# Performance work log

Hardware: AMD Instinct MI355X
Metric: run time of the kernel (lower is better)

The kernel has to match this reference:

```python
import jax, jax.numpy as jnp
import numpy as np

B, T, C = 4, 2048, 1024
H = 16
HD = C // H  # 64
OBS_DIM, ACT_DIM = 17, 6
JOINED_DIM = OBS_DIM + ACT_DIM + 2  # 25


def _make_mask():
    # tril causal mask with every (JOINED_DIM-1 + k*JOINED_DIM)-th column zeroed (RL branch)
    m = np.tril(np.ones((T, T), dtype=np.float32))
    m[:, JOINED_DIM - 1::JOINED_DIM] = 0.0
    return jnp.asarray(m > 0)  # bool [T, T]


MASK = _make_mask()


def setup_inputs() -> dict:
    key = jax.random.key(0)
    ks = jax.random.split(key, 9)
    s = 1.0 / np.sqrt(C)
    return {
        "x": jax.random.normal(ks[0], (B, T, C), dtype=jnp.float32),
        "Wq": jax.random.normal(ks[1], (C, C), dtype=jnp.float32) * s,
        "bq": jax.random.normal(ks[2], (C,), dtype=jnp.float32) * s,
        "Wk": jax.random.normal(ks[3], (C, C), dtype=jnp.float32) * s,
        "bk": jax.random.normal(ks[4], (C,), dtype=jnp.float32) * s,
        "Wv": jax.random.normal(ks[5], (C, C), dtype=jnp.float32) * s,
        "bv": jax.random.normal(ks[6], (C,), dtype=jnp.float32) * s,
        "Wp": jax.random.normal(ks[7], (C, C), dtype=jnp.float32) * s,
        "bp": jax.random.normal(ks[8], (C,), dtype=jnp.float32) * s,
    }


def reference(x, Wq, bq, Wk, bk, Wv, bv, Wp, bp):
    # torch nn.Linear: y = x @ W.T + b
    def split_heads(t):  # [B,T,C] -> [B,H,T,HD]
        return t.reshape(B, T, H, HD).transpose(0, 2, 1, 3)

    q = split_heads(x @ Wq.T + bq)
    k = split_heads(x @ Wk.T + bk)
    v = split_heads(x @ Wv.T + bv)

    att = jnp.einsum("bhqd,bhkd->bhqk", q, k) * (1.0 / np.sqrt(HD))
    att = jnp.where(MASK[None, None, :, :], att, -jnp.inf)
    att = jax.nn.softmax(att, axis=-1)
    # dropout layers are identity in eval mode

    y = jnp.einsum("bhqk,bhkd->bhqd", att, v)  # [B,H,T,HD]
    y = y.transpose(0, 2, 1, 3).reshape(B, T, C)
    return y @ Wp.T + bp
```

## Files before the change

### kernel.cpp

```cpp
#include <hip/hip_runtime.h>
#include <hip/hip_bf16.h>


typedef __attribute__((ext_vector_type(8))) short short8;
typedef __attribute__((ext_vector_type(4))) float floatx4;
typedef unsigned short us;

__device__ __forceinline__ us f2bf(float f){
    union { __hip_bfloat16 h; us u; } cv;
    cv.h = __float2bfloat16(f);
    return cv.u;
}

__device__ __forceinline__ void ld_g2l16(const void* g, void* l){
    __builtin_amdgcn_global_load_lds((const __attribute__((address_space(1))) void*)g,
                                     (__attribute__((address_space(3))) void*)l, 16, 0, 0);
}

__global__ __launch_bounds__(256) void cvt_kernel(const float* __restrict__ in,
                                                  us* __restrict__ out, int n4){
    int i = blockIdx.x * 256 + threadIdx.x;
    if (i < n4){
        float4 v = reinterpret_cast<const float4*>(in)[i];
        ushort4 o;
        o.x = f2bf(v.x); o.y = f2bf(v.y); o.z = f2bf(v.z); o.w = f2bf(v.w);
        reinterpret_cast<ushort4*>(out)[i] = o;
    }
}

__global__ __launch_bounds__(256) void cvt4_kernel(const float* __restrict__ w0, const float* __restrict__ w1,
                                                   const float* __restrict__ w2, const float* __restrict__ w3,
                                                   us* __restrict__ o0, us* __restrict__ o1,
                                                   us* __restrict__ o2, us* __restrict__ o3){
    int wsel = blockIdx.x >> 10;
    int i = (blockIdx.x & 1023) * 256 + threadIdx.x;
    const float* src = (wsel == 0) ? w0 : (wsel == 1) ? w1 : (wsel == 2) ? w2 : w3;
    us* dst = (wsel == 0) ? o0 : (wsel == 1) ? o1 : (wsel == 2) ? o2 : o3;
    float4 v = reinterpret_cast<const float4*>(src)[i];
    ushort4 o;
    o.x = f2bf(v.x); o.y = f2bf(v.y); o.z = f2bf(v.z); o.w = f2bf(v.w);
    reinterpret_cast<ushort4*>(dst)[i] = o;
}


#define QSCALE 0.1803368801111244f

#define BAR() __builtin_amdgcn_s_barrier()
#define LGKM0() do { asm volatile("s_waitcnt lgkmcnt(0)" ::: "memory"); __builtin_amdgcn_sched_barrier(0); } while(0)
#define VMC6() asm volatile("s_waitcnt vmcnt(6)" ::: "memory")
#define VMC0() asm volatile("s_waitcnt vmcnt(0)" ::: "memory")

#define STAGE_A3(buf, kt) do { \
    _Pragma("unroll") \
    for (int c_ = 0; c_ < 4; c_++) \
        ld_g2l16(A + (size_t)(m0 + srow[c_])*1024 + (kt)*64 + sgr[c_]*8, \
                 &smem[(buf)*24576 + (c_*8 + wave)*512]); \
} while(0)

#define STAGE_B3(buf, kt) do { \
    _Pragma("unroll") \
    for (int c_ = 0; c_ < 2; c_++) \
        ld_g2l16(Wb + (size_t)(n0 + srow[c_])*1024 + (kt)*64 + sgr[c_]*8, \
                 &smem[(buf)*24576 + 16384 + (c_*8 + wave)*512]); \
} while(0)

#define LOAD_AF3(buf, IH) do { \
    _Pragma("unroll") \
    for (int i_ = 0; i_ < 4; i_++){ \
        int ra_ = wm*128 + (IH)*64 + i_*16 + lane15; \
        _Pragma("unroll") \
        for (int ks_ = 0; ks_ < 2; ks_++){ \
            int ga_ = (ks_*4 + quad) ^ (ra_ & 7); \
            af[i_][ks_] = *reinterpret_cast<const short8*>(&smem[(buf)*24576 + ra_*64 + ga_*8]); \
        } } \
} while(0)

#define LOAD_BF3(buf) do { \
    _Pragma("unroll") \
    for (int j_ = 0; j_ < 2; j_++){ \
        int rb_ = wn*32 + j_*16 + lane15; \
        _Pragma("unroll") \
        for (int ks_ = 0; ks_ < 2; ks_++){ \
            int gb_ = (ks_*4 + quad) ^ (rb_ & 7); \
            bf[j_][ks_] = *reinterpret_cast<const short8*>(&smem[(buf)*24576 + 16384 + rb_*64 + gb_*8]); \
        } } \
} while(0)

#define MFMA_PH3(IH) do { \
    __builtin_amdgcn_s_setprio(1); \
    _Pragma("unroll") \
    for (int ks_ = 0; ks_ < 2; ks_++) \
        _Pragma("unroll") \
        for (int i_ = 0; i_ < 4; i_++) \
            _Pragma("unroll") \
            for (int j_ = 0; j_ < 2; j_++) \
                acc[(IH)*4 + i_][j_] = __builtin_amdgcn_mfma_f32_16x16x32_bf16( \
                    af[i_][ks_], bf[j_][ks_], acc[(IH)*4 + i_][j_], 0, 0, 0); \
    __builtin_amdgcn_s_setprio(0); \
} while(0)

__global__ __launch_bounds__(512, 2) void gemm_qkv3(
    const us* __restrict__ A,
    const us* __restrict__ Wqb, const us* __restrict__ Wkb, const us* __restrict__ Wvb,
    const float* __restrict__ bq, const float* __restrict__ bk, const float* __restrict__ bv,
    us* __restrict__ qo, us* __restrict__ ko, us* __restrict__ vto)
{
    __shared__ us smem[73728];
    const int tid = threadIdx.x;
    const int lane = tid & 63;
    const int wave = tid >> 6;
    const int lane15 = lane & 15;
    const int quad = lane >> 4;
    const int wm = wave >> 2;
    const int wn = wave & 3;
    const int seg = blockIdx.x >> 3;
    const int n0 = (blockIdx.x & 7) * 128;
    const int m0 = blockIdx.y * 256;

    const us* Wb = (seg == 0) ? Wqb : (seg == 1) ? Wkb : Wvb;
    const float* bias = (seg == 0) ? bq : (seg == 1) ? bk : bv;

    int srow[4], sgr[4];
    #pragma unroll
    for (int c = 0; c < 4; c++){
        int s = (c*8 + wave)*64 + lane;
        srow[c] = s >> 3;
        sgr[c] = (s & 7) ^ ((s >> 3) & 7);
    }

    floatx4 zero = {0.f, 0.f, 0.f, 0.f};
    floatx4 acc[8][2];
    #pragma unroll
    for (int i = 0; i < 8; i++)
        #pragma unroll
        for (int j = 0; j < 2; j++) acc[i][j] = zero;
    short8 af[4][2];
    short8 bf[2][2];

    STAGE_A3(0, 0); STAGE_B3(0, 0);
    STAGE_A3(1, 1); STAGE_B3(1, 1);
    VMC6(); BAR();

    #pragma unroll
    for (int t = 0; t < 16; t++){
        const int cur = t % 3, nxt = (t + 2) % 3;
        LOAD_AF3(cur, 0); LOAD_BF3(cur);
        if (t < 14) STAGE_A3(nxt, t + 2);
        BAR(); LGKM0();
        MFMA_PH3(0);
        BAR();
        LOAD_AF3(cur, 1);
        if (t < 14) STAGE_B3(nxt, t + 2);
        BAR(); LGKM0();
        MFMA_PH3(1);
        if (t < 14) { VMC6(); } else { VMC0(); }
        BAR();
    }

    if (seg < 2){
        #pragma unroll
        for (int i = 0; i < 8; i++){
            #pragma unroll
            for (int j = 0; j < 2; j++){
                int n = n0 + wn*32 + j*16 + lane15;
                float bvv = bias[n];
                #pragma unroll
                for (int r = 0; r < 4; r++){
                    int m = m0 + wm*128 + i*16 + quad*4 + r;
                    float val = acc[i][j][r] + bvv;
                    if (seg == 0){
                        qo[(size_t)m*1024 + n] = f2bf(val * QSCALE);
                    } else {
                        int b = m >> 11, tt = m & 2047;
                        int h = n >> 6,  d = n & 63;
                        ko[(((size_t)b*16 + h)*2048 + tt)*64 + d] = f2bf(val);
                    }
                }
            }
        }
    } else {
        us* lCT = smem;
        const int b = m0 >> 11;
        const int t0 = m0 & 2047;
        #pragma unroll
        for (int j = 0; j < 2; j++){
            int nl = wn*32 + j*16 + lane15;
            float bvv = bias[n0 + nl];
            #pragma unroll
            for (int i = 0; i < 8; i++){
                int ml = wm*128 + i*16 + quad*4;
                unsigned int lo = (unsigned int)f2bf(acc[i][j][0] + bvv) |
                                  ((unsigned int)f2bf(acc[i][j][1] + bvv) << 16);
                unsigned int hi = (unsigned int)f2bf(acc[i][j][2] + bvv) |
                                  ((unsigned int)f2bf(acc[i][j][3] + bvv) << 16);
                uint2 pk2; pk2.x = lo; pk2.y = hi;
                *reinterpret_cast<uint2*>(&lCT[(size_t)nl*264 + ml]) = pk2;
            }
        }
        __syncthreads();
        int nl = tid >> 2;
        int c4 = tid & 3;
        int nC = n0 + nl;
        int h = nC >> 6, d = nC & 63;
        us* dst = vto + (((size_t)b*16 + h)*64 + d)*2048 + t0 + c4*64;
        #pragma unroll
        for (int ii = 0; ii < 8; ii++){
            uint4 v = *reinterpret_cast<const uint4*>(&lCT[(size_t)nl*264 + c4*64 + ii*8]);
            *reinterpret_cast<uint4*>(dst + ii*8) = v;
        }
    }
}

__device__ __forceinline__ void pstore_rg(
    floatx4 (&s)[4], us* pw, bool diag, int rgrow, int j0, int jr, const int (&res)[4],
    int lane15, int quad)
{
    #pragma unroll
    for (int tj = 0; tj < 4; tj++){
        bool bad = (res[tj] + jr) == 24;
        #pragma unroll
        for (int r = 0; r < 4; r++){
            float p = __builtin_amdgcn_exp2f(s[tj][r]);
            bool kill = bad || (diag && (j0 + tj*16 + lane15 > rgrow + quad*4 + r));
            pw[(quad*4 + r)*72 + tj*16 + lane15] = f2bf(kill ? 0.f : p);
        }
    }
}

__global__ __launch_bounds__(256, 3) void flash_attn(
    const us* __restrict__ q,
    const us* __restrict__ k,
    const us* __restrict__ vT,
    us* __restrict__ y)
{
    __shared__ us lK[2][64*64];
    __shared__ us lV[2][64*64];
    __shared__ us lP[4][2][16*72];
    const int tid = threadIdx.x;
    const int lane = tid & 63;
    const int wave = tid >> 6;
    const int lane15 = lane & 15;
    const int quad = lane >> 4;
    const int lin = blockIdx.x;
    const int qt2 = 15 - (lin >> 6);
    const int bh = lin & 63;
    const int b = bh >> 4, h = bh & 15;
    const int rg0 = qt2*128 + wave*16;
    const int rg1 = rg0 + 64;
    const int nIter = 2*qt2 + 2;

    const us* kb = k  + (size_t)bh*2048*64;
    const us* vb = vT + (size_t)bh*64*2048;

    const us* q0 = q + ((size_t)b*2048 + rg0 + lane15)*1024 + h*64 + quad*8;
    const us* q1 = q + ((size_t)b*2048 + rg1 + lane15)*1024 + h*64 + quad*8;
    short8 qf0a = *reinterpret_cast<const short8*>(q0);
    short8 qf0b = *reinterpret_cast<const short8*>(q0 + 32);
    short8 qf1a = *reinterpret_cast<const short8*>(q1);
    short8 qf1b = *reinterpret_cast<const short8*>(q1 + 32);

    floatx4 zero = {0.f, 0.f, 0.f, 0.f};
    floatx4 acc0[4], acc1[4];
    #pragma unroll
    for (int d = 0; d < 4; d++){ acc0[d] = zero; acc1[d] = zero; }
    floatx4 lacc0 = zero, lacc1 = zero;

    us* pw0 = &lP[wave][0][0];
    us* pw1 = &lP[wave][1][0];

    short8 onesb;
    #pragma unroll
    for (int e = 0; e < 8; e++) onesb[e] = (short)0x3F80;

    int res[4];
    #pragma unroll
    for (int tj = 0; tj < 4; tj++) res[tj] = (tj*16 + lane15) % 25;
    int jr = 0;

    int srow[2], sgr[2];
    #pragma unroll
    for (int i = 0; i < 2; i++){
        int s = (i*4 + wave)*64 + lane;
        srow[i] = s >> 3;
        sgr[i] = (s & 7) ^ ((s >> 3) & 7);
    }

    #pragma unroll
    for (int i = 0; i < 2; i++){
        ld_g2l16(kb + (size_t)srow[i]*64 + sgr[i]*8, &lK[0][(i*4 + wave)*512]);
        ld_g2l16(vb + (size_t)srow[i]*2048 + sgr[i]*8, &lV[0][(i*4 + wave)*512]);
    }

    for (int it = 0; it < nIter; it++){
        const int j0 = it*64;
        __syncthreads();

        if (it + 1 < nIter){
            #pragma unroll
            for (int i = 0; i < 2; i++){
                ld_g2l16(kb + (size_t)(j0 + 64 + srow[i])*64 + sgr[i]*8,
                         &lK[(it + 1) & 1][(i*4 + wave)*512]);
                ld_g2l16(vb + (size_t)srow[i]*2048 + j0 + 64 + sgr[i]*8,
                         &lV[(it + 1) & 1][(i*4 + wave)*512]);
            }
        }

        const us* Kb = lK[it & 1];
        const us* Vb = lV[it & 1];
        const bool act0  = (it + 1 < nIter);
        const bool diag0 = (it + 2 == nIter);
        const bool diag1 = (it + 1 == nIter);

        floatx4 s0[4], s1[4];
        #pragma unroll
        for (int tj = 0; tj < 4; tj++){
            int rk = tj*16 + lane15;
            short8 kf0 = *reinterpret_cast<const short8*>(&Kb[rk*64 + ((quad     ^ (rk & 7)))*8]);
            short8 kf1 = *reinterpret_cast<const short8*>(&Kb[rk*64 + (((4+quad) ^ (rk & 7)))*8]);
            floatx4 z1 = __builtin_amdgcn_mfma_f32_16x16x32_bf16(qf1a, kf0, zero, 0, 0, 0);
            s1[tj]     = __builtin_amdgcn_mfma_f32_16x16x32_bf16(qf1b, kf1, z1,   0, 0, 0);
            if (act0){
                floatx4 z0 = __builtin_amdgcn_mfma_f32_16x16x32_bf16(qf0a, kf0, zero, 0, 0, 0);
                s0[tj]     = __builtin_amdgcn_mfma_f32_16x16x32_bf16(qf0b, kf1, z0,   0, 0, 0);
            }
        }

        pstore_rg(s1, pw1, diag1, rg1, j0, jr, res, lane15, quad);
        if (act0)
            pstore_rg(s0, pw0, diag0, rg0, j0, jr, res, lane15, quad);

        #pragma unroll
        for (int ks = 0; ks < 2; ks++){
            short8 pf1 = *reinterpret_cast<const short8*>(&pw1[lane15*72 + ks*32 + quad*8]);
            short8 pf0 = *reinterpret_cast<const short8*>(&pw0[lane15*72 + ks*32 + quad*8]);
            lacc1 = __builtin_amdgcn_mfma_f32_16x16x32_bf16(pf1, onesb, lacc1, 0, 0, 0);
            if (act0) lacc0 = __builtin_amdgcn_mfma_f32_16x16x32_bf16(pf0, onesb, lacc0, 0, 0, 0);
            #pragma unroll
            for (int dt = 0; dt < 4; dt++){
                int rv = dt*16 + lane15;
                short8 vf = *reinterpret_cast<const short8*>(&Vb[rv*64 + (((ks*4+quad) ^ (rv & 7)))*8]);
                acc1[dt] = __builtin_amdgcn_mfma_f32_16x16x32_bf16(pf1, vf, acc1[dt], 0, 0, 0);
                if (act0) acc0[dt] = __builtin_amdgcn_mfma_f32_16x16x32_bf16(pf0, vf, acc0[dt], 0, 0, 0);
            }
        }

        jr += 14; if (jr >= 25) jr -= 25;
    }

    float rl0[4], rl1[4];
    #pragma unroll
    for (int r = 0; r < 4; r++){ rl0[r] = 1.0f / lacc0[r]; rl1[r] = 1.0f / lacc1[r]; }
    #pragma unroll
    for (int dt = 0; dt < 4; dt++){
        #pragma unroll
        for (int r = 0; r < 4; r++){
            int t0 = rg0 + quad*4 + r;
            int t1 = rg1 + quad*4 + r;
            int cc = h*64 + dt*16 + lane15;
            y[((size_t)b*2048 + t0)*1024 + cc] = f2bf(acc0[dt][r] * rl0[r]);
            y[((size_t)b*2048 + t1)*1024 + cc] = f2bf(acc1[dt][r] * rl1[r]);
        }
    }
}

__global__ __launch_bounds__(256) void gemm_out(
    const us* __restrict__ A,
    const us* __restrict__ Wb,
    const float* __restrict__ bias,
    float* __restrict__ out)
{
    __shared__ us lA[128*64];
    __shared__ us lB[128*64];
    const int tid = threadIdx.x;
    const int lane = tid & 63;
    const int wave = tid >> 6;
    const int lane15 = lane & 15;
    const int quad = lane >> 4;
    const int wm = wave >> 1, wn = wave & 1;
    const int m0 = blockIdx.y * 128;
    const int n0 = blockIdx.x * 128;

    floatx4 zero = {0.f, 0.f, 0.f, 0.f};
    floatx4 acc[4][4];
    #pragma unroll
    for (int i = 0; i < 4; i++)
        #pragma unroll
        for (int j = 0; j < 4; j++) acc[i][j] = zero;

    int srow[4], sg[4];
    #pragma unroll
    for (int t = 0; t < 4; t++){
        int s = (t*4 + wave)*64 + lane;
        srow[t] = s >> 3;
        sg[t] = (s & 7) ^ ((s >> 3) & 7);
    }

    for (int k0 = 0; k0 < 1024; k0 += 64){
        #pragma unroll
        for (int t = 0; t < 4; t++){
            int chunk = t*4 + wave;
            ld_g2l16(A  + (size_t)(m0 + srow[t])*1024 + k0 + sg[t]*8, &lA[chunk*512]);
            ld_g2l16(Wb + (size_t)(n0 + srow[t])*1024 + k0 + sg[t]*8, &lB[chunk*512]);
        }
        __syncthreads();
        #pragma unroll
        for (int ks = 0; ks < 2; ks++){
            short8 af[4], bf[4];
            #pragma unroll
            for (int i = 0; i < 4; i++){
                int ra = wm*64 + i*16 + lane15;
                int ga = (ks*4 + quad) ^ (ra & 7);
                af[i] = *reinterpret_cast<const short8*>(&lA[ra*64 + ga*8]);
                int rb = wn*64 + i*16 + lane15;
                int gb = (ks*4 + quad) ^ (rb & 7);
                bf[i] = *reinterpret_cast<const short8*>(&lB[rb*64 + gb*8]);
            }
            #pragma unroll
            for (int i = 0; i < 4; i++)
                #pragma unroll
                for (int j = 0; j < 4; j++)
                    acc[i][j] = __builtin_amdgcn_mfma_f32_16x16x32_bf16(af[i], bf[j], acc[i][j], 0, 0, 0);
        }
        __syncthreads();
    }

    #pragma unroll
    for (int i = 0; i < 4; i++){
        #pragma unroll
        for (int j = 0; j < 4; j++){
            int n = n0 + wn*64 + j*16 + lane15;
            float bvv = bias[n];
            #pragma unroll
            for (int r = 0; r < 4; r++){
                int m = m0 + wm*64 + i*16 + quad*4 + r;
                out[(size_t)m*1024 + n] = acc[i][j][r] + bvv;
            }
        }
    }
}

extern "C" void kernel_launch(void* const* d_in, const int* in_sizes, int n_in,
                              void* d_out, int out_size, void* d_ws, size_t ws_size,
                              hipStream_t stream)
{
    const float* x  = (const float*)d_in[0];
    const float* Wq = (const float*)d_in[1];
    const float* bq = (const float*)d_in[2];
    const float* Wk = (const float*)d_in[3];
    const float* bk = (const float*)d_in[4];
    const float* Wv = (const float*)d_in[5];
    const float* bv = (const float*)d_in[6];
    const float* Wp = (const float*)d_in[7];
    const float* bp = (const float*)d_in[8];
    float* out = (float*)d_out;

    us* ws  = (us*)d_ws;
    us* xbf = ws;
    us* wqb = xbf + (size_t)8192*1024;
    us* wkb = wqb + (size_t)1024*1024;
    us* wvb = wkb + (size_t)1024*1024;
    us* wpb = wvb + (size_t)1024*1024;
    us* qws = wpb + (size_t)1024*1024;
    us* kws = qws + (size_t)8388608;
    us* vtw = kws + (size_t)8388608;
    us* yws = vtw + (size_t)8388608;

    cvt_kernel<<<8192, 256, 0, stream>>>(x, xbf, 2097152);
    cvt4_kernel<<<4096, 256, 0, stream>>>(Wq, Wk, Wv, Wp, wqb, wkb, wvb, wpb);

    gemm_qkv3<<<dim3(24, 32), 512, 0, stream>>>(xbf, wqb, wkb, wvb, bq, bk, bv, qws, kws, vtw);

    flash_attn<<<1024, 256, 0, stream>>>(qws, kws, vtw, yws);

    gemm_out<<<dim3(8, 64), 256, 0, stream>>>(yws, wpb, bp, out);
}
```

Measured before the change: 263.3 us.

## Pair attention tiles per block, move mask into V and row-sum, pipeline output GEMM

The attention kernel now has each block handle two query tiles (g and 15-g), which balances causal work across 512 blocks. It also splits the loop into specialised full and diagonal bodies. The periodic column mask moves out of the inner loop: masked V columns are zeroed when V^T is written, and a bf16 mask vector replaces the all-ones operand in the row-sum MFMA. The P buffer pitch changes from 72 to 68, and P is read as two 8-byte halves. The output projection reuses the triple-buffered 256x128 pipelined GEMM macros from the QKV kernel in place of the simple single-buffer version. The risks are a longer serial loop per block and bank conflicts from the new pitch.

```diff
diff --git a/kernel.cpp b/kernel.cpp
--- a/kernel.cpp
+++ b/kernel.cpp
@@ -3,6 +3,7 @@
 
 
 typedef __attribute__((ext_vector_type(8))) short short8;
+typedef __attribute__((ext_vector_type(4))) short short4v;
 typedef __attribute__((ext_vector_type(4))) float floatx4;
 typedef unsigned short us;
 
@@ -53,7 +54,7 @@
 #define STAGE_A3(buf, kt) do { \
     _Pragma("unroll") \
     for (int c_ = 0; c_ < 4; c_++) \
-        ld_g2l16(A + (size_t)(m0 + srow[c_])*1024 + (kt)*64 + sgr[c_]*8, \
+        ld_g2l16(Ag + (size_t)(m0 + srow[c_])*1024 + (kt)*64 + sgr[c_]*8, \
                  &smem[(buf)*24576 + (c_*8 + wave)*512]); \
 } while(0)
 
@@ -100,7 +101,7 @@
 } while(0)
 
 __global__ __launch_bounds__(512, 2) void gemm_qkv3(
-    const us* __restrict__ A,
+    const us* __restrict__ Ag,
     const us* __restrict__ Wqb, const us* __restrict__ Wkb, const us* __restrict__ Wvb,
     const float* __restrict__ bq, const float* __restrict__ bk, const float* __restrict__ bv,
     us* __restrict__ qo, us* __restrict__ ko, us* __restrict__ vto)
@@ -203,29 +204,100 @@
         int nC = n0 + nl;
         int h = nC >> 6, d = nC & 63;
         us* dst = vto + (((size_t)b*16 + h)*64 + d)*2048 + t0 + c4*64;
+        int rr = (t0 + c4*64) % 25;
         #pragma unroll
         for (int ii = 0; ii < 8; ii++){
             uint4 v = *reinterpret_cast<const uint4*>(&lCT[(size_t)nl*264 + c4*64 + ii*8]);
+            us* pv = reinterpret_cast<us*>(&v);
+            #pragma unroll
+            for (int e = 0; e < 8; e++){
+                if (rr == 24) pv[e] = 0;
+                rr = (rr == 24) ? 0 : rr + 1;
+            }
             *reinterpret_cast<uint4*>(dst + ii*8) = v;
         }
     }
 }
 
-__device__ __forceinline__ void pstore_rg(
-    floatx4 (&s)[4], us* pw, bool diag, int rgrow, int j0, int jr, const int (&res)[4],
-    int lane15, int quad)
-{
+
+__device__ __forceinline__ short8 rdP(const us* pw, int lane15, int ks, int quad){
+    const us* a = &pw[lane15*68 + ks*32 + quad*8];
+    short4v lo = *reinterpret_cast<const short4v*>(a);
+    short4v hi = *reinterpret_cast<const short4v*>(a + 4);
+    short8 r = {lo[0], lo[1], lo[2], lo[3], hi[0], hi[1], hi[2], hi[3]};
+    return r;
+}
+
+__device__ __forceinline__ void pstore_plain(floatx4 (&s)[4], us* pw, int lane15, int quad){
+    #pragma unroll
+    for (int tj = 0; tj < 4; tj++)
+        #pragma unroll
+        for (int r = 0; r < 4; r++)
+            pw[(quad*4 + r)*68 + tj*16 + lane15] = f2bf(__builtin_amdgcn_exp2f(s[tj][r]));
+}
+
+__device__ __forceinline__ void pstore_diag(floatx4 (&s)[4], us* pw, int rgrow, int j0,
+                                            int lane15, int quad){
     #pragma unroll
     for (int tj = 0; tj < 4; tj++){
-        bool bad = (res[tj] + jr) == 24;
         #pragma unroll
         for (int r = 0; r < 4; r++){
             float p = __builtin_amdgcn_exp2f(s[tj][r]);
-            bool kill = bad || (diag && (j0 + tj*16 + lane15 > rgrow + quad*4 + r));
-            pw[(quad*4 + r)*72 + tj*16 + lane15] = f2bf(kill ? 0.f : p);
-        }
-    }
-}
+            bool kill = (j0 + tj*16 + lane15) > (rgrow + quad*4 + r);
+            pw[(quad*4 + r)*68 + tj*16 + lane15] = f2bf(kill ? 0.f : p);
+        }
+    }
+}
+
+#define ATT_STAGE(itn) do { \
+    _Pragma("unroll") \
+    for (int i_ = 0; i_ < 2; i_++){ \
+        ld_g2l16(kb + (size_t)((itn)*64 + srow[i_])*64 + sgr[i_]*8, &lK[(itn) & 1][(i_*4 + wave)*512]); \
+        ld_g2l16(vb + (size_t)srow[i_]*2048 + (itn)*64 + sgr[i_]*8, &lV[(itn) & 1][(i_*4 + wave)*512]); \
+    } } while(0)
+
+#define ATT_BODY(MODE, ITV) do { \
+    const int j0_ = (ITV)*64; \
+    __syncthreads(); \
+    if ((ITV) + 1 < nIter) ATT_STAGE((ITV) + 1); \
+    const us* Kb = lK[(ITV) & 1]; \
+    const us* Vb = lV[(ITV) & 1]; \
+    floatx4 s0[4], s1[4]; \
+    _Pragma("unroll") \
+    for (int tj = 0; tj < 4; tj++){ \
+        int rk = tj*16 + lane15; \
+        short8 kf0 = *reinterpret_cast<const short8*>(&Kb[rk*64 + ((quad     ^ (rk & 7)))*8]); \
+        short8 kf1 = *reinterpret_cast<const short8*>(&Kb[rk*64 + (((4+quad) ^ (rk & 7)))*8]); \
+        floatx4 z1 = __builtin_amdgcn_mfma_f32_16x16x32_bf16(qf1a, kf0, zero, 0, 0, 0); \
+        s1[tj]     = __builtin_amdgcn_mfma_f32_16x16x32_bf16(qf1b, kf1, z1,   0, 0, 0); \
+        if ((MODE) != 2){ \
+            floatx4 z0 = __builtin_amdgcn_mfma_f32_16x16x32_bf16(qf0a, kf0, zero, 0, 0, 0); \
+            s0[tj]     = __builtin_amdgcn_mfma_f32_16x16x32_bf16(qf0b, kf1, z0,   0, 0, 0); \
+        } \
+    } \
+    if ((MODE) == 2)      pstore_diag(s1, pw1, rg1, j0_, lane15, quad); \
+    else                  pstore_plain(s1, pw1, lane15, quad); \
+    if ((MODE) == 1)      pstore_diag(s0, pw0, rg0, j0_, lane15, quad); \
+    else if ((MODE) == 0) pstore_plain(s0, pw0, lane15, quad); \
+    _Pragma("unroll") \
+    for (int ks = 0; ks < 2; ks++){ \
+        short8 mfr = *reinterpret_cast<const short8*>(&lmask[j0_ + ks*32 + quad*8]); \
+        short8 pf1 = rdP(pw1, lane15, ks, quad); \
+        short8 pf0; \
+        lacc1 = __builtin_amdgcn_mfma_f32_16x16x32_bf16(pf1, mfr, lacc1, 0, 0, 0); \
+        if ((MODE) != 2){ \
+            pf0 = rdP(pw0, lane15, ks, quad); \
+            lacc0 = __builtin_amdgcn_mfma_f32_16x16x32_bf16(pf0, mfr, lacc0, 0, 0, 0); \
+        } \
+        _Pragma("unroll") \
+        for (int dt = 0; dt < 4; dt++){ \
+            int rv = dt*16 + lane15; \
+            short8 vf = *reinterpret_cast<const short8*>(&Vb[rv*64 + (((ks*4+quad) ^ (rv & 7)))*8]); \
+            acc1[dt] = __builtin_amdgcn_mfma_f32_16x16x32_bf16(pf1, vf, acc1[dt], 0, 0, 0); \
+            if ((MODE) != 2) acc0[dt] = __builtin_amdgcn_mfma_f32_16x16x32_bf16(pf0, vf, acc0[dt], 0, 0, 0); \
+        } \
+    } \
+} while(0)
 
 __global__ __launch_bounds__(256, 3) void flash_attn(
     const us* __restrict__ q,
@@ -235,47 +307,37 @@
 {
     __shared__ us lK[2][64*64];
     __shared__ us lV[2][64*64];
-    __shared__ us lP[4][2][16*72];
+    __shared__ us lP[4][2][16*68];
+    __shared__ us lmask[2048];
     const int tid = threadIdx.x;
     const int lane = tid & 63;
     const int wave = tid >> 6;
     const int lane15 = lane & 15;
     const int quad = lane >> 4;
     const int lin = blockIdx.x;
-    const int qt2 = 15 - (lin >> 6);
+    const int g  = lin >> 6;
     const int bh = lin & 63;
     const int b = bh >> 4, h = bh & 15;
-    const int rg0 = qt2*128 + wave*16;
-    const int rg1 = rg0 + 64;
-    const int nIter = 2*qt2 + 2;
 
     const us* kb = k  + (size_t)bh*2048*64;
     const us* vb = vT + (size_t)bh*64*2048;
 
-    const us* q0 = q + ((size_t)b*2048 + rg0 + lane15)*1024 + h*64 + quad*8;
-    const us* q1 = q + ((size_t)b*2048 + rg1 + lane15)*1024 + h*64 + quad*8;
-    short8 qf0a = *reinterpret_cast<const short8*>(q0);
-    short8 qf0b = *reinterpret_cast<const short8*>(q0 + 32);
-    short8 qf1a = *reinterpret_cast<const short8*>(q1);
-    short8 qf1b = *reinterpret_cast<const short8*>(q1 + 32);
+    {
+        int c0 = tid * 8;
+        int rr = c0 % 25;
+        ushort4 mv[2];
+        us* pm = reinterpret_cast<us*>(mv);
+        #pragma unroll
+        for (int e = 0; e < 8; e++){
+            pm[e] = (rr == 24) ? (us)0 : (us)0x3F80;
+            rr = (rr == 24) ? 0 : rr + 1;
+        }
+        *reinterpret_cast<uint4*>(&lmask[c0]) = *reinterpret_cast<uint4*>(mv);
+    }
 
     floatx4 zero = {0.f, 0.f, 0.f, 0.f};
-    floatx4 acc0[4], acc1[4];
-    #pragma unroll
-    for (int d = 0; d < 4; d++){ acc0[d] = zero; acc1[d] = zero; }
-    floatx4 lacc0 = zero, lacc1 = zero;
-
     us* pw0 = &lP[wave][0][0];
     us* pw1 = &lP[wave][1][0];
-
-    short8 onesb;
-    #pragma unroll
-    for (int e = 0; e < 8; e++) onesb[e] = (short)0x3F80;
-
-    int res[4];
-    #pragma unroll
-    for (int tj = 0; tj < 4; tj++) res[tj] = (tj*16 + lane15) % 25;
-    int jr = 0;
 
     int srow[2], sgr[2];
     #pragma unroll
@@ -285,154 +347,113 @@
         sgr[i] = (s & 7) ^ ((s >> 3) & 7);
     }
 
-    #pragma unroll
-    for (int i = 0; i < 2; i++){
-        ld_g2l16(kb + (size_t)srow[i]*64 + sgr[i]*8, &lK[0][(i*4 + wave)*512]);
-        ld_g2l16(vb + (size_t)srow[i]*2048 + sgr[i]*8, &lV[0][(i*4 + wave)*512]);
-    }
-
-    for (int it = 0; it < nIter; it++){
-        const int j0 = it*64;
-        __syncthreads();
-
-        if (it + 1 < nIter){
+    #pragma unroll 1
+    for (int pass = 0; pass < 2; pass++){
+        const int qt2 = pass ? (15 - g) : g;
+        const int rg0 = qt2*128 + wave*16;
+        const int rg1 = rg0 + 64;
+        const int nIter = 2*qt2 + 2;
+
+        const us* q0 = q + ((size_t)b*2048 + rg0 + lane15)*1024 + h*64 + quad*8;
+        const us* q1 = q + ((size_t)b*2048 + rg1 + lane15)*1024 + h*64 + quad*8;
+        short8 qf0a = *reinterpret_cast<const short8*>(q0);
+        short8 qf0b = *reinterpret_cast<const short8*>(q0 + 32);
+        short8 qf1a = *reinterpret_cast<const short8*>(q1);
+        short8 qf1b = *reinterpret_cast<const short8*>(q1 + 32);
+
+        floatx4 acc0[4], acc1[4];
+        #pragma unroll
+        for (int d = 0; d < 4; d++){ acc0[d] = zero; acc1[d] = zero; }
+        floatx4 lacc0 = zero, lacc1 = zero;
+
+        ATT_STAGE(0);
+
+        int it = 0;
+        #pragma unroll 1
+        for (; it < nIter - 2; it++) ATT_BODY(0, it);
+        ATT_BODY(1, it); it++;
+        ATT_BODY(2, it);
+
+        float rl0[4], rl1[4];
+        #pragma unroll
+        for (int r = 0; r < 4; r++){ rl0[r] = 1.0f / lacc0[r]; rl1[r] = 1.0f / lacc1[r]; }
+        #pragma unroll
+        for (int dt = 0; dt < 4; dt++){
             #pragma unroll
-            for (int i = 0; i < 2; i++){
-                ld_g2l16(kb + (size_t)(j0 + 64 + srow[i])*64 + sgr[i]*8,
-                         &lK[(it + 1) & 1][(i*4 + wave)*512]);
-                ld_g2l16(vb + (size_t)srow[i]*2048 + j0 + 64 + sgr[i]*8,
-                         &lV[(it + 1) & 1][(i*4 + wave)*512]);
+            for (int r = 0; r < 4; r++){
+                int t0 = rg0 + quad*4 + r;
+                int t1 = rg1 + quad*4 + r;
+                int cc = h*64 + dt*16 + lane15;
+                y[((size_t)b*2048 + t0)*1024 + cc] = f2bf(acc0[dt][r] * rl0[r]);
+                y[((size_t)b*2048 + t1)*1024 + cc] = f2bf(acc1[dt][r] * rl1[r]);
             }
         }
-
-        const us* Kb = lK[it & 1];
-        const us* Vb = lV[it & 1];
-        const bool act0  = (it + 1 < nIter);
-        const bool diag0 = (it + 2 == nIter);
-        const bool diag1 = (it + 1 == nIter);
-
-        floatx4 s0[4], s1[4];
-        #pragma unroll
-        for (int tj = 0; tj < 4; tj++){
-            int rk = tj*16 + lane15;
-            short8 kf0 = *reinterpret_cast<const short8*>(&Kb[rk*64 + ((quad     ^ (rk & 7)))*8]);
-            short8 kf1 = *reinterpret_cast<const short8*>(&Kb[rk*64 + (((4+quad) ^ (rk & 7)))*8]);
-            floatx4 z1 = __builtin_amdgcn_mfma_f32_16x16x32_bf16(qf1a, kf0, zero, 0, 0, 0);
-            s1[tj]     = __builtin_amdgcn_mfma_f32_16x16x32_bf16(qf1b, kf1, z1,   0, 0, 0);
-            if (act0){
-                floatx4 z0 = __builtin_amdgcn_mfma_f32_16x16x32_bf16(qf0a, kf0, zero, 0, 0, 0);
-                s0[tj]     = __builtin_amdgcn_mfma_f32_16x16x32_bf16(qf0b, kf1, z0,   0, 0, 0);
-            }
-        }
-
-        pstore_rg(s1, pw1, diag1, rg1, j0, jr, res, lane15, quad);
-        if (act0)
-            pstore_rg(s0, pw0, diag0, rg0, j0, jr, res, lane15, quad);
-
-        #pragma unroll
-        for (int ks = 0; ks < 2; ks++){
-            short8 pf1 = *reinterpret_cast<const short8*>(&pw1[lane15*72 + ks*32 + quad*8]);
-            short8 pf0 = *reinterpret_cast<const short8*>(&pw0[lane15*72 + ks*32 + quad*8]);
-            lacc1 = __builtin_amdgcn_mfma_f32_16x16x32_bf16(pf1, onesb, lacc1, 0, 0, 0);
-            if (act0) lacc0 = __builtin_amdgcn_mfma_f32_16x16x32_bf16(pf0, onesb, lacc0, 0, 0, 0);
-            #pragma unroll
-            for (int dt = 0; dt < 4; dt++){
-                int rv = dt*16 + lane15;
-                short8 vf = *reinterpret_cast<const short8*>(&Vb[rv*64 + (((ks*4+quad) ^ (rv & 7)))*8]);
-                acc1[dt] = __builtin_amdgcn_mfma_f32_16x16x32_bf16(pf1, vf, acc1[dt], 0, 0, 0);
-                if (act0) acc0[dt] = __builtin_amdgcn_mfma_f32_16x16x32_bf16(pf0, vf, acc0[dt], 0, 0, 0);
-            }
-        }
-
-        jr += 14; if (jr >= 25) jr -= 25;
-    }
-
-    float rl0[4], rl1[4];
-    #pragma unroll
-    for (int r = 0; r < 4; r++){ rl0[r] = 1.0f / lacc0[r]; rl1[r] = 1.0f / lacc1[r]; }
-    #pragma unroll
-    for (int dt = 0; dt < 4; dt++){
-        #pragma unroll
-        for (int r = 0; r < 4; r++){
-            int t0 = rg0 + quad*4 + r;
-            int t1 = rg1 + quad*4 + r;
-            int cc = h*64 + dt*16 + lane15;
-            y[((size_t)b*2048 + t0)*1024 + cc] = f2bf(acc0[dt][r] * rl0[r]);
-            y[((size_t)b*2048 + t1)*1024 + cc] = f2bf(acc1[dt][r] * rl1[r]);
-        }
-    }
-}
-
-__global__ __launch_bounds__(256) void gemm_out(
-    const us* __restrict__ A,
+    }
+}
+
+__global__ __launch_bounds__(512, 2) void gemm_out3(
+    const us* __restrict__ Ag,
     const us* __restrict__ Wb,
     const float* __restrict__ bias,
     float* __restrict__ out)
 {
-    __shared__ us lA[128*64];
-    __shared__ us lB[128*64];
+    __shared__ us smem[73728];
     const int tid = threadIdx.x;
     const int lane = tid & 63;
     const int wave = tid >> 6;
     const int lane15 = lane & 15;
     const int quad = lane >> 4;
-    const int wm = wave >> 1, wn = wave & 1;
-    const int m0 = blockIdx.y * 128;
+    const int wm = wave >> 2;
+    const int wn = wave & 3;
     const int n0 = blockIdx.x * 128;
+    const int m0 = blockIdx.y * 256;
+
+    int srow[4], sgr[4];
+    #pragma unroll
+    for (int c = 0; c < 4; c++){
+        int s = (c*8 + wave)*64 + lane;
+        srow[c] = s >> 3;
+        sgr[c] = (s & 7) ^ ((s >> 3) & 7);
+    }
 
     floatx4 zero = {0.f, 0.f, 0.f, 0.f};
-    floatx4 acc[4][4];
-    #pragma unroll
-    for (int i = 0; i < 4; i++)
-        #pragma unroll
-        for (int j = 0; j < 4; j++) acc[i][j] = zero;
-
-    int srow[4], sg[4];
-    #pragma unroll
-    for (int t = 0; t < 4; t++){
-        int s = (t*4 + wave)*64 + lane;
-        srow[t] = s >> 3;
-        sg[t] = (s & 7) ^ ((s >> 3) & 7);
-    }
-
-    for (int k0 = 0; k0 < 1024; k0 += 64){
-        #pragma unroll
-        for (int t = 0; t < 4; t++){
-            int chunk = t*4 + wave;
-            ld_g2l16(A  + (size_t)(m0 + srow[t])*1024 + k0 + sg[t]*8, &lA[chunk*512]);
-            ld_g2l16(Wb + (size_t)(n0 + srow[t])*1024 + k0 + sg[t]*8, &lB[chunk*512]);
-        }
-        __syncthreads();
-        #pragma unroll
-        for (int ks = 0; ks < 2; ks++){
-            short8 af[4], bf[4];
-            #pragma unroll
-            for (int i = 0; i < 4; i++){
-                int ra = wm*64 + i*16 + lane15;
-                int ga = (ks*4 + quad) ^ (ra & 7);
-                af[i] = *reinterpret_cast<const short8*>(&lA[ra*64 + ga*8]);
-                int rb = wn*64 + i*16 + lane15;
-                int gb = (ks*4 + quad) ^ (rb & 7);
-                bf[i] = *reinterpret_cast<const short8*>(&lB[rb*64 + gb*8]);
-            }
-            #pragma unroll
-            for (int i = 0; i < 4; i++)
-                #pragma unroll
-                for (int j = 0; j < 4; j++)
-                    acc[i][j] = __builtin_amdgcn_mfma_f32_16x16x32_bf16(af[i], bf[j], acc[i][j], 0, 0, 0);
-        }
-        __syncthreads();
-    }
-
-    #pragma unroll
-    for (int i = 0; i < 4; i++){
-        #pragma unroll
-        for (int j = 0; j < 4; j++){
-            int n = n0 + wn*64 + j*16 + lane15;
+    floatx4 acc[8][2];
+    #pragma unroll
+    for (int i = 0; i < 8; i++)
+        #pragma unroll
+        for (int j = 0; j < 2; j++) acc[i][j] = zero;
+    short8 af[4][2];
+    short8 bf[2][2];
+
+    STAGE_A3(0, 0); STAGE_B3(0, 0);
+    STAGE_A3(1, 1); STAGE_B3(1, 1);
+    VMC6(); BAR();
+
+    #pragma unroll
+    for (int t = 0; t < 16; t++){
+        const int cur = t % 3, nxt = (t + 2) % 3;
+        LOAD_AF3(cur, 0); LOAD_BF3(cur);
+        if (t < 14) STAGE_A3(nxt, t + 2);
+        BAR(); LGKM0();
+        MFMA_PH3(0);
+        BAR();
+        LOAD_AF3(cur, 1);
+        if (t < 14) STAGE_B3(nxt, t + 2);
+        BAR(); LGKM0();
+        MFMA_PH3(1);
+        if (t < 14) { VMC6(); } else { VMC0(); }
+        BAR();
+    }
+
+    #pragma unroll
+    for (int i = 0; i < 8; i++){
+        #pragma unroll
+        for (int j = 0; j < 2; j++){
+            int n = n0 + wn*32 + j*16 + lane15;
             float bvv = bias[n];
             #pragma unroll
             for (int r = 0; r < 4; r++){
-                int m = m0 + wm*64 + i*16 + quad*4 + r;
+                int m = m0 + wm*128 + i*16 + quad*4 + r;
                 out[(size_t)m*1024 + n] = acc[i][j][r] + bvv;
             }
         }
@@ -470,7 +491,7 @@
 
     gemm_qkv3<<<dim3(24, 32), 512, 0, stream>>>(xbf, wqb, wkb, wvb, bq, bk, bv, qws, kws, vtw);
 
-    flash_attn<<<1024, 256, 0, stream>>>(qws, kws, vtw, yws);
-
-    gemm_out<<<dim3(8, 64), 256, 0, stream>>>(yws, wpb, bp, out);
-}
+    flash_attn<<<512, 256, 0, stream>>>(qws, kws, vtw, yws);
+
+    gemm_out3<<<dim3(8, 32), 512, 0, stream>>>(yws, wpb, bp, out);
+}
```

After: 256.7 us. 2.5% less time.
